# Kernel optimization log

Measured on AMD Instinct MI355X. Metric: run time of the kernel, lower is better.

## Reference

```python
import jax, jax.numpy as jnp
import numpy as np

V, ENC, D, E = 10000, 2048, 512, 512
B, L = 128, 64


def setup_inputs() -> dict:
    key = jax.random.key(0)
    ks = jax.random.split(key, 12)
    s = lambda *sh: 1.0 / np.sqrt(sh[-1])
    return {
        "global_feats": jax.random.normal(ks[0], (B, ENC), jnp.float32),
        "encoded_captions": jax.random.randint(ks[1], (B, L), 0, V, jnp.int64),
        "caption_lengths": jax.random.randint(ks[2], (B,), 1, L, jnp.int64),
        "W_embed": jax.random.normal(ks[3], (V, E), jnp.float32) * 0.02,
        "W_init": jax.random.normal(ks[4], (D, ENC), jnp.float32) * s(ENC),
        "b_init": jnp.zeros((D,), jnp.float32),
        "W_ih": jax.random.normal(ks[5], (3 * D, E), jnp.float32) * s(E),
        "W_hh": jax.random.normal(ks[6], (3 * D, D), jnp.float32) * s(D),
        "b_ih": jnp.zeros((3 * D,), jnp.float32),
        "b_hh": jnp.zeros((3 * D,), jnp.float32),
        "W_fc": jax.random.normal(ks[7], (V, D), jnp.float32) * s(D),
        "b_fc": jnp.zeros((V,), jnp.float32),
    }


def reference(global_feats, encoded_captions, caption_lengths,
              W_embed, W_init, b_init, W_ih, W_hh, b_ih, b_hh, W_fc, b_fc):
    # init_hidden: h0 = tanh(Linear(global_feats))  -> (B, D)
    h0 = jnp.tanh(global_feats @ W_init.T + b_init)

    # teacher forcing over timesteps 0..L-2 (PyTorch GRU gate order: r, z, n)
    emb = W_embed[encoded_captions[:, : L - 1]]          # (B, L-1, E)
    gi = jnp.einsum('ble,ge->blg', emb, W_ih) + b_ih     # (B, L-1, 3D) precomputed input gates
    gi = jnp.swapaxes(gi, 0, 1)                          # (L-1, B, 3D) scan over time

    def step(h, gi_t):
        gh = h @ W_hh.T + b_hh                           # (B, 3D)
        i_r, i_z, i_n = jnp.split(gi_t, 3, axis=-1)
        h_r, h_z, h_n = jnp.split(gh, 3, axis=-1)
        r = jax.nn.sigmoid(i_r + h_r)
        z = jax.nn.sigmoid(i_z + h_z)
        n = jnp.tanh(i_n + r * h_n)
        h_new = (1.0 - z) * n + z * h
        return h_new, h_new

    _, hs = jax.lax.scan(step, h0, gi)                   # hs: (L-1, B, D)
    # dropout is identity in eval/reference mode
    logits = jnp.einsum('lbd,vd->blv', hs, W_fc) + b_fc  # (B, L-1, V)
    return logits, caption_lengths - 1
```

## Files before the change

kernel.cpp:

```cpp
#include <hip/hip_runtime.h>
#include <hip/hip_bf16.h>

#define V_    10000
#define ENC_  2048
#define D_    512
#define B_    128
#define L_    64
#define T_    63
#define M_    (B_ * L_ - B_)
#define G_    (3 * D_)
#define LOGITS_SZ ((long)M_ * V_)
#define SCAN_NB 64

typedef __bf16 bf16x8_t __attribute__((ext_vector_type(8)));
typedef float  f32x4_t  __attribute__((ext_vector_type(4)));
typedef short  s16x8_t  __attribute__((ext_vector_type(8)));
typedef unsigned long long ull_t;

typedef __attribute__((address_space(3))) char*       lds_cptr_t;
typedef const __attribute__((address_space(1))) char* glb_cptr_t;

__device__ __forceinline__ void gload_lds16(const void* g, void* l) {
  __builtin_amdgcn_global_load_lds((glb_cptr_t)g, (lds_cptr_t)l, 16, 0, 0);
}
__device__ __forceinline__ float bf2f(short s) {
  return __uint_as_float(((unsigned)(unsigned short)s) << 16);
}
__device__ __forceinline__ short f2bf(float f) {
  __hip_bfloat16 h = __float2bfloat16(f);
  return *reinterpret_cast<short*>(&h);
}
__device__ __forceinline__ s16x8_t cvt8(const float* p) {
  f32x4_t lo = *reinterpret_cast<const f32x4_t*>(p);
  f32x4_t hi = *reinterpret_cast<const f32x4_t*>(p + 4);
  s16x8_t r;
#pragma unroll
  for (int e = 0; e < 4; e++) { r[e] = f2bf(lo[e]); r[4 + e] = f2bf(hi[e]); }
  return r;
}
__device__ __forceinline__ float sigmoidf_(float x) {
  return 1.0f / (1.0f + __expf(-x));
}
__device__ __forceinline__ bf16x8_t lds_frag(const short* p) {
  return __builtin_bit_cast(bf16x8_t, *reinterpret_cast<const s16x8_t*>(p));
}

__global__ void GG_cvt5(const float* __restrict__ whh, __hip_bfloat16* __restrict__ dwhh,
                        const float* __restrict__ wih, __hip_bfloat16* __restrict__ dwih,
                        const float* __restrict__ wemb, __hip_bfloat16* __restrict__ dwemb,
                        const float* __restrict__ winit, __hip_bfloat16* __restrict__ dwinit,
                        const float* __restrict__ gf, __hip_bfloat16* __restrict__ dgf) {
  const int i = blockIdx.x * blockDim.x + threadIdx.x;
  const float* s; __hip_bfloat16* d; int off;
  if (i < 98304)        { s = whh;   d = dwhh;   off = i; }
  else if (i < 196608)  { s = wih;   d = dwih;   off = i - 98304; }
  else if (i < 836608)  { s = wemb;  d = dwemb;  off = i - 196608; }
  else if (i < 967680)  { s = winit; d = dwinit; off = i - 836608; }
  else                  { s = gf;    d = dgf;    off = i - 967680; }
  s16x8_t v = cvt8(s + (long)off * 8);
  *reinterpret_cast<s16x8_t*>(d + (long)off * 8) = v;
}

__global__ void GG_cvt_kernel(const float* __restrict__ src,
                              __hip_bfloat16* __restrict__ dst, int n8) {
  int i = blockIdx.x * blockDim.x + threadIdx.x;
  if (i < n8) {
    s16x8_t v = cvt8(src + (long)i * 8);
    *reinterpret_cast<s16x8_t*>(dst + (long)i * 8) = v;
  }
}

__global__ __launch_bounds__(256) void GG_gemm_h0(
    const __hip_bfloat16* __restrict__ gfB,
    const __hip_bfloat16* __restrict__ WinitB,
    const float* __restrict__ binit,
    __hip_bfloat16* __restrict__ hfull) {
  __shared__ short sA[128 * 64];
  __shared__ short sB[128 * 64];
  const int lane = threadIdx.x & 63;
  const int wave = threadIdx.x >> 6;
  const int n0 = blockIdx.x * 128;
  const int srow = lane >> 3;
  const int scol = (lane & 7) * 8;

  f32x4_t acc[4][4] = {};

  const __hip_bfloat16* aptr[4];
  const __hip_bfloat16* bptr[4];
#pragma unroll
  for (int i = 0; i < 4; i++) {
    const int r = (wave * 4 + i) * 8 + srow;
    aptr[i] = gfB + (long)r * ENC_ + scol;
    bptr[i] = WinitB + (long)(n0 + r) * ENC_ + scol;
  }

  const int wm = (wave >> 1) * 64;
  const int wn = (wave & 1) * 64;
  const int fr = lane & 15;
  const int fk = (lane >> 4) * 8;

  for (int kt = 0; kt < 32; kt++) {
    __syncthreads();
#pragma unroll
    for (int i = 0; i < 4; i++) {
      const int chunk = wave * 4 + i;
      gload_lds16(aptr[i] + kt * 64, sA + chunk * 512);
      gload_lds16(bptr[i] + kt * 64, sB + chunk * 512);
    }
    __syncthreads();
#pragma unroll
    for (int kk = 0; kk < 2; kk++) {
      bf16x8_t a[4], b[4];
#pragma unroll
      for (int i = 0; i < 4; i++) {
        a[i] = lds_frag(sA + (wm + i * 16 + fr) * 64 + kk * 32 + fk);
        b[i] = lds_frag(sB + (wn + i * 16 + fr) * 64 + kk * 32 + fk);
      }
#pragma unroll
      for (int i = 0; i < 4; i++)
#pragma unroll
        for (int j = 0; j < 4; j++)
          acc[i][j] = __builtin_amdgcn_mfma_f32_16x16x32_bf16(a[i], b[j], acc[i][j], 0, 0, 0);
    }
  }

  const int fq = lane >> 4;
#pragma unroll
  for (int j = 0; j < 4; j++) {
    const int n = n0 + wn + j * 16 + fr;
    const float bv = binit[n];
#pragma unroll
    for (int i = 0; i < 4; i++)
#pragma unroll
      for (int rr = 0; rr < 4; rr++) {
        const int m = wm + i * 16 + fq * 4 + rr;
        hfull[(long)m * 64 * 512 + n] = __float2bfloat16(tanhf(acc[i][j][rr] + bv));
      }
  }
}

__global__ __launch_bounds__(256) void GG_gemm_gi(
    const __hip_bfloat16* __restrict__ WembB,
    const int* __restrict__ cap,
    const __hip_bfloat16* __restrict__ WihB,
    const float* __restrict__ bias,
    __hip_bfloat16* __restrict__ C) {
  __shared__ short sA[128 * 64];
  __shared__ short sB[128 * 64];
  const int lane = threadIdx.x & 63;
  const int wave = threadIdx.x >> 6;
  const int m0 = blockIdx.y * 128;
  const int n0 = blockIdx.x * 128;
  const int srow = lane >> 3;
  const int scol = (lane & 7) * 8;

  f32x4_t acc[4][4] = {};

  const __hip_bfloat16* aptr[4];
  const __hip_bfloat16* bptr[4];
#pragma unroll
  for (int i = 0; i < 4; i++) {
    const int r = (wave * 4 + i) * 8 + srow;
    const int bt = m0 + r;
    const int bb = bt / 63;
    const int tt = bt - bb * 63;
    aptr[i] = WembB + (long)cap[bb * L_ + tt] * 512 + scol;
    bptr[i] = WihB + (long)(n0 + r) * 512 + scol;
  }

  const int wm = (wave >> 1) * 64;
  const int wn = (wave & 1) * 64;
  const int fr = lane & 15;
  const int fk = (lane >> 4) * 8;

  for (int kt = 0; kt < 8; kt++) {
    __syncthreads();
#pragma unroll
    for (int i = 0; i < 4; i++) {
      const int chunk = wave * 4 + i;
      gload_lds16(aptr[i] + kt * 64, sA + chunk * 512);
      gload_lds16(bptr[i] + kt * 64, sB + chunk * 512);
    }
    __syncthreads();
#pragma unroll
    for (int kk = 0; kk < 2; kk++) {
      bf16x8_t a[4], b[4];
#pragma unroll
      for (int i = 0; i < 4; i++) {
        a[i] = lds_frag(sA + (wm + i * 16 + fr) * 64 + kk * 32 + fk);
        b[i] = lds_frag(sB + (wn + i * 16 + fr) * 64 + kk * 32 + fk);
      }
#pragma unroll
      for (int i = 0; i < 4; i++)
#pragma unroll
        for (int j = 0; j < 4; j++)
          acc[i][j] = __builtin_amdgcn_mfma_f32_16x16x32_bf16(a[i], b[j], acc[i][j], 0, 0, 0);
    }
  }

  const int fq = lane >> 4;
#pragma unroll
  for (int j = 0; j < 4; j++) {
    const int n = n0 + wn + j * 16 + fr;
    const float bv = bias[n];
#pragma unroll
    for (int i = 0; i < 4; i++)
#pragma unroll
      for (int rr = 0; rr < 4; rr++) {
        const int m = m0 + wm + i * 16 + fq * 4 + rr;
        C[(long)m * G_ + n] = __float2bfloat16(acc[i][j][rr] + bv);
      }
  }
}

template <bool BBF16>
__global__ __launch_bounds__(512) void GG_gemm_logits(
    const __hip_bfloat16* __restrict__ hfull,
    const void* __restrict__ Bsrc,
    const float* __restrict__ bias,
    float* __restrict__ C) {
  const int flat = blockIdx.x;
  const int xcd = flat & 7;
  const int s = flat >> 3;
  const int col = xcd * 5 + s % 5;
  const int row = s / 5;
  const int m0 = row * 128;
  const int n0 = col * 256;

  __shared__ short sA[128 * 64];
  __shared__ short sB[256 * 64];
  const int lane = threadIdx.x & 63;
  const int wave = threadIdx.x >> 6;
  const int srow = lane >> 3;
  const int scol = (lane & 7) * 8;

  f32x4_t acc[4][4] = {};

  const __hip_bfloat16* aptr[2];
#pragma unroll
  for (int i = 0; i < 2; i++) {
    const int r = (wave + i * 8) * 8 + srow;
    const int m = m0 + r;
    const int bb = m / 63;
    const int tt = m - bb * 63;
    aptr[i] = hfull + ((long)bb * 64 + tt + 1) * 512 + scol;
  }
  const __hip_bfloat16* bptrB[4];
  const float* bptrF[4];
#pragma unroll
  for (int i = 0; i < 4; i++) {
    int nrow = n0 + (wave + i * 8) * 8 + srow;
    nrow = (nrow < V_) ? nrow : (V_ - 1);
    if constexpr (BBF16) bptrB[i] = (const __hip_bfloat16*)Bsrc + (long)nrow * 512 + scol;
    else                 bptrF[i] = (const float*)Bsrc + (long)nrow * 512 + scol;
  }

  const int wm = (wave >> 2) * 64;
  const int wn = (wave & 3) * 64;
  const int fr = lane & 15;
  const int fk = (lane >> 4) * 8;

  for (int kt = 0; kt < 8; kt++) {
    s16x8_t vb[4];
    if constexpr (!BBF16) {
#pragma unroll
      for (int i = 0; i < 4; i++) vb[i] = cvt8(bptrF[i] + kt * 64);
    }
    __syncthreads();
#pragma unroll
    for (int i = 0; i < 2; i++)
      gload_lds16(aptr[i] + kt * 64, sA + (wave + i * 8) * 512);
#pragma unroll
    for (int i = 0; i < 4; i++) {
      if constexpr (BBF16)
        gload_lds16(bptrB[i] + kt * 64, sB + (wave + i * 8) * 512);
      else
        *reinterpret_cast<s16x8_t*>(sB + (wave + i * 8) * 512 + lane * 8) = vb[i];
    }
    __syncthreads();
#pragma unroll
    for (int kk = 0; kk < 2; kk++) {
      bf16x8_t a[4], b[4];
#pragma unroll
      for (int i = 0; i < 4; i++) {
        a[i] = lds_frag(sA + (wm + i * 16 + fr) * 64 + kk * 32 + fk);
        b[i] = lds_frag(sB + (wn + i * 16 + fr) * 64 + kk * 32 + fk);
      }
#pragma unroll
      for (int i = 0; i < 4; i++)
#pragma unroll
        for (int j = 0; j < 4; j++)
          acc[i][j] = __builtin_amdgcn_mfma_f32_16x16x32_bf16(a[i], b[j], acc[i][j], 0, 0, 0);
    }
  }

  const int fq = lane >> 4;
#pragma unroll
  for (int j = 0; j < 4; j++) {
    const int n = n0 + wn + j * 16 + fr;
    if (n >= V_) continue;
    const float bv = bias[n];
#pragma unroll
    for (int i = 0; i < 4; i++)
#pragma unroll
      for (int rr = 0; rr < 4; rr++) {
        const int m = m0 + wm + i * 16 + fq * 4 + rr;
        C[(long)m * V_ + n] = acc[i][j][rr] + bv;
      }
  }
}

__global__ __launch_bounds__(256) void GG_scan_persist(
    __hip_bfloat16* __restrict__ hfull,
    const __hip_bfloat16* __restrict__ gi,
    const __hip_bfloat16* __restrict__ WhhB,
    const float* __restrict__ bhh,
    int* __restrict__ flagbase) {
  __shared__ short sW[48 * 512];
  const int lane = threadIdx.x & 63;
  const int wave = threadIdx.x >> 6;
  const int strip = blockIdx.x & 31;
  const int half  = blockIdx.x >> 5;
  const int d0 = strip * 16;
  const int fr = lane & 15;
  const int g4 = lane >> 4;
  int* myflags = flagbase + half * 32;

  for (int rr = wave; rr < 48; rr += 4) {
    const int grow = (rr >> 4) * 512 + d0 + (rr & 15);
    gload_lds16(WhhB + (long)grow * 512 + (lane ^ (rr & 7)) * 8, sW + rr * 512);
  }

  const int dd = d0 + fr;
  const int bbase = half * 64 + wave * 16 + g4 * 4;
  const float br_ = bhh[dd], bz_ = bhh[512 + dd], bn_ = bhh[1024 + dd];
  const short* gis = (const short*)gi;

  const int arow = half * 64 + wave * 16 + fr;
  const ull_t abase0 =
      (ull_t)hfull + ((ull_t)arow * 64 * 512 + (unsigned)(g4 * 8)) * 2ull;

  ull_t sbase[4];
  const short* gp0[4];
#pragma unroll
  for (int rr = 0; rr < 4; rr++) {
    sbase[rr] = (ull_t)hfull +
                ((ull_t)(bbase + rr) * 64 * 512 + (unsigned)dd) * 2ull;
    gp0[rr] = gis + (long)(bbase + rr) * T_ * G_ + dd;
  }

  unsigned cr[4], cz[4], cn[4];
  float hp[4];
#pragma unroll
  for (int rr = 0; rr < 4; rr++) {
    cr[rr] = (unsigned short)gp0[rr][0];
    cz[rr] = (unsigned short)gp0[rr][512];
    cn[rr] = (unsigned short)gp0[rr][1024];
    hp[rr] = bf2f(*(const short*)&hfull[((long)(bbase + rr) * 64) * 512 + dd]);
  }

  asm volatile("s_waitcnt vmcnt(0)" ::: "memory");
  __syncthreads();

  for (int t = 0; t < T_; t++) {
    if (t > 0) {
      while (true) {
        const int v = __hip_atomic_load(&myflags[lane & 31], __ATOMIC_RELAXED,
                                        __HIP_MEMORY_SCOPE_SYSTEM);
        if (__all(v >= t)) break;
        __builtin_amdgcn_s_sleep(1);
      }
    }

    const ull_t ab = abase0 + (ull_t)t * 1024ull;
    f32x4_t a[16];
#define ALOAD(IDX, OFF)                                                        \
    asm volatile("global_load_dwordx4 %0, %1, off offset:" #OFF " sc0 sc1"     \
                 : "=v"(a[IDX]) : "v"(ab));
    ALOAD(0, 0)    ALOAD(1, 64)   ALOAD(2, 128)  ALOAD(3, 192)
    ALOAD(4, 256)  ALOAD(5, 320)  ALOAD(6, 384)  ALOAD(7, 448)
    ALOAD(8, 512)  ALOAD(9, 576)  ALOAD(10, 640) ALOAD(11, 704)
    ALOAD(12, 768) ALOAD(13, 832) ALOAD(14, 896) ALOAD(15, 960)
#undef ALOAD

    const int tp = (t < T_ - 1) ? (t + 1) : (T_ - 1);
    unsigned nr[4], nz[4], nn[4];
#pragma unroll
    for (int rr = 0; rr < 4; rr++) {
      const short* gp = gp0[rr] + (long)tp * G_;
      asm volatile("global_load_ushort %0, %1, off"             : "=v"(nr[rr]) : "v"(gp));
      asm volatile("global_load_ushort %0, %1, off offset:1024" : "=v"(nz[rr]) : "v"(gp));
      asm volatile("global_load_ushort %0, %1, off offset:2048" : "=v"(nn[rr]) : "v"(gp));
    }

    asm volatile("s_waitcnt vmcnt(12)" ::: "memory");
    __builtin_amdgcn_sched_barrier(0);

    f32x4_t acc[3] = {};
#pragma unroll
    for (int kt = 0; kt < 16; kt++) {
      const bf16x8_t afr = __builtin_bit_cast(bf16x8_t, a[kt]);
      const int gsw = ((kt * 4 + g4) ^ (fr & 7)) * 8;
      bf16x8_t bfr[3];
#pragma unroll
      for (int j = 0; j < 3; j++) bfr[j] = lds_frag(sW + (j * 16 + fr) * 512 + gsw);
#pragma unroll
      for (int j = 0; j < 3; j++)
        acc[j] = __builtin_amdgcn_mfma_f32_16x16x32_bf16(afr, bfr[j], acc[j], 0, 0, 0);
    }

#pragma unroll
    for (int rr = 0; rr < 4; rr++) {
      const float rg = sigmoidf_(bf2f((short)cr[rr]) + acc[0][rr] + br_);
      const float zg = sigmoidf_(bf2f((short)cz[rr]) + acc[1][rr] + bz_);
      const float ng = tanhf(bf2f((short)cn[rr]) + rg * (acc[2][rr] + bn_));
      const short hnb = f2bf((1.f - zg) * ng + zg * hp[rr]);
      hp[rr] = bf2f(hnb);
      const ull_t saddr = sbase[rr] + (ull_t)(t + 1) * 1024ull;
      const unsigned int val = (unsigned short)hnb;
      asm volatile("global_store_short %0, %1, off sc0 sc1"
                   :: "v"(saddr), "v"(val) : "memory");
    }

    asm volatile("s_waitcnt vmcnt(0)" ::: "memory");
    __builtin_amdgcn_sched_barrier(0);
#pragma unroll
    for (int rr = 0; rr < 4; rr++) { cr[rr] = nr[rr]; cz[rr] = nz[rr]; cn[rr] = nn[rr]; }

    if (t < T_ - 1) {
      __syncthreads();
      if (threadIdx.x == 0)
        __hip_atomic_store(&myflags[strip], t + 1, __ATOMIC_RELAXED,
                           __HIP_MEMORY_SCOPE_SYSTEM);
    }
  }
}

__global__ void GG_tail_kernel(const int* __restrict__ lens, float* __restrict__ out) {
  const int b = threadIdx.x;
  if (b < B_) out[LOGITS_SZ + b] = (float)(lens[b] - 1);
}

extern "C" void kernel_launch(void* const* d_in, const int* in_sizes, int n_in,
                              void* d_out, int out_size, void* d_ws, size_t ws_size,
                              hipStream_t stream) {
  const float* gf      = (const float*)d_in[0];
  const int*   cap     = (const int*)d_in[1];
  const int*   lens    = (const int*)d_in[2];
  const float* W_embed = (const float*)d_in[3];
  const float* W_init  = (const float*)d_in[4];
  const float* b_init  = (const float*)d_in[5];
  const float* W_ih    = (const float*)d_in[6];
  const float* W_hh    = (const float*)d_in[7];
  const float* b_ih    = (const float*)d_in[8];
  const float* b_hh    = (const float*)d_in[9];
  const float* W_fc    = (const float*)d_in[10];
  const float* b_fc    = (const float*)d_in[11];
  float* out = (float*)d_out;

  char* ob = (char*)d_out;
  __hip_bfloat16* gi_ws  = (__hip_bfloat16*)ob;
  __hip_bfloat16* WhhB   = (__hip_bfloat16*)(ob + 25165824);
  __hip_bfloat16* WihB   = (__hip_bfloat16*)(ob + 27262976);
  __hip_bfloat16* WembB  = (__hip_bfloat16*)(ob + 29360128);
  __hip_bfloat16* WinitB = (__hip_bfloat16*)(ob + 40894464);
  __hip_bfloat16* gfB    = (__hip_bfloat16*)(ob + 43253760);

  __hip_bfloat16* hfull = (__hip_bfloat16*)d_ws;
  __hip_bfloat16* WfcB  = (__hip_bfloat16*)((char*)d_ws + 8388608);
  const bool big_ws = ws_size >= (size_t)(8388608 + 10240000 + 256);
  int* flags = (int*)((char*)d_ws + (big_ws ? 18628608 : 8388608));

  hipMemsetAsync(flags, 0, 256, stream);

  GG_cvt5<<<dim3(3908), 256, 0, stream>>>(W_hh, WhhB, W_ih, WihB, W_embed, WembB,
                                          W_init, WinitB, gf, gfB);
  if (big_ws)
    GG_cvt_kernel<<<dim3((V_ * D_ / 8 + 255) / 256), 256, 0, stream>>>(W_fc, WfcB, V_ * D_ / 8);

  GG_gemm_h0<<<dim3(4), 256, 0, stream>>>(gfB, WinitB, b_init, hfull);

  GG_gemm_gi<<<dim3(G_ / 128, M_ / 128), 256, 0, stream>>>(WembB, cap, WihB, b_ih, gi_ws);

  GG_scan_persist<<<dim3(SCAN_NB), 256, 0, stream>>>(hfull, gi_ws, WhhB, b_hh, flags);

  if (big_ws)
    GG_gemm_logits<true><<<dim3(2520), 512, 0, stream>>>(hfull, WfcB, b_fc, out);
  else
    GG_gemm_logits<false><<<dim3(2520), 512, 0, stream>>>(hfull, W_fc, b_fc, out);

  GG_tail_kernel<<<dim3(1), 128, 0, stream>>>(lens, out);
}
```

Baseline: 543.2 us.

## XOR-swizzle LDS tiles in GEMMs and fold W_fc conversion into one kernel

Applies an XOR swizzle to the 16-byte column chunks of the LDS tiles in the h0, gi and logits GEMMs. Global-to-LDS loads write permuted chunks and fragment reads use the matching XOR index, which is meant to cut LDS bank conflicts on the MFMA fragment reads. It also merges the separate W_fc fp32-to-bf16 conversion launch into the existing multi-tensor conversion kernel, saving one launch. The swizzle must line up exactly between writers and readers on both the gload_lds and the register-store paths.

```diff
diff --git a/kernel.cpp b/kernel.cpp
--- a/kernel.cpp
+++ b/kernel.cpp
@@ -45,29 +45,25 @@
   return __builtin_bit_cast(bf16x8_t, *reinterpret_cast<const s16x8_t*>(p));
 }
 
-__global__ void GG_cvt5(const float* __restrict__ whh, __hip_bfloat16* __restrict__ dwhh,
+__global__ void GG_cvt6(const float* __restrict__ whh, __hip_bfloat16* __restrict__ dwhh,
                         const float* __restrict__ wih, __hip_bfloat16* __restrict__ dwih,
                         const float* __restrict__ wemb, __hip_bfloat16* __restrict__ dwemb,
                         const float* __restrict__ winit, __hip_bfloat16* __restrict__ dwinit,
-                        const float* __restrict__ gf, __hip_bfloat16* __restrict__ dgf) {
+                        const float* __restrict__ gf, __hip_bfloat16* __restrict__ dgf,
+                        const float* __restrict__ wfc, __hip_bfloat16* __restrict__ dwfc) {
   const int i = blockIdx.x * blockDim.x + threadIdx.x;
   const float* s; __hip_bfloat16* d; int off;
   if (i < 98304)        { s = whh;   d = dwhh;   off = i; }
   else if (i < 196608)  { s = wih;   d = dwih;   off = i - 98304; }
   else if (i < 836608)  { s = wemb;  d = dwemb;  off = i - 196608; }
   else if (i < 967680)  { s = winit; d = dwinit; off = i - 836608; }
-  else                  { s = gf;    d = dgf;    off = i - 967680; }
+  else if (i < 1000448) { s = gf;    d = dgf;    off = i - 967680; }
+  else {
+    if (dwfc == nullptr || i >= 1640448) return;
+    s = wfc; d = dwfc; off = i - 1000448;
+  }
   s16x8_t v = cvt8(s + (long)off * 8);
   *reinterpret_cast<s16x8_t*>(d + (long)off * 8) = v;
-}
-
-__global__ void GG_cvt_kernel(const float* __restrict__ src,
-                              __hip_bfloat16* __restrict__ dst, int n8) {
-  int i = blockIdx.x * blockDim.x + threadIdx.x;
-  if (i < n8) {
-    s16x8_t v = cvt8(src + (long)i * 8);
-    *reinterpret_cast<s16x8_t*>(dst + (long)i * 8) = v;
-  }
 }
 
 __global__ __launch_bounds__(256) void GG_gemm_h0(
@@ -81,7 +77,7 @@
   const int wave = threadIdx.x >> 6;
   const int n0 = blockIdx.x * 128;
   const int srow = lane >> 3;
-  const int scol = (lane & 7) * 8;
+  const int scolz = ((lane & 7) ^ (srow & 7)) * 8;
 
   f32x4_t acc[4][4] = {};
 
@@ -90,14 +86,14 @@
 #pragma unroll
   for (int i = 0; i < 4; i++) {
     const int r = (wave * 4 + i) * 8 + srow;
-    aptr[i] = gfB + (long)r * ENC_ + scol;
-    bptr[i] = WinitB + (long)(n0 + r) * ENC_ + scol;
+    aptr[i] = gfB + (long)r * ENC_ + scolz;
+    bptr[i] = WinitB + (long)(n0 + r) * ENC_ + scolz;
   }
 
   const int wm = (wave >> 1) * 64;
   const int wn = (wave & 1) * 64;
   const int fr = lane & 15;
-  const int fk = (lane >> 4) * 8;
+  const int g4 = lane >> 4;
 
   for (int kt = 0; kt < 32; kt++) {
     __syncthreads();
@@ -110,11 +106,12 @@
     __syncthreads();
 #pragma unroll
     for (int kk = 0; kk < 2; kk++) {
+      const int gsw = ((kk * 4 + g4) ^ (fr & 7)) * 8;
       bf16x8_t a[4], b[4];
 #pragma unroll
       for (int i = 0; i < 4; i++) {
-        a[i] = lds_frag(sA + (wm + i * 16 + fr) * 64 + kk * 32 + fk);
-        b[i] = lds_frag(sB + (wn + i * 16 + fr) * 64 + kk * 32 + fk);
+        a[i] = lds_frag(sA + (wm + i * 16 + fr) * 64 + gsw);
+        b[i] = lds_frag(sB + (wn + i * 16 + fr) * 64 + gsw);
       }
 #pragma unroll
       for (int i = 0; i < 4; i++)
@@ -152,7 +149,7 @@
   const int m0 = blockIdx.y * 128;
   const int n0 = blockIdx.x * 128;
   const int srow = lane >> 3;
-  const int scol = (lane & 7) * 8;
+  const int scolz = ((lane & 7) ^ (srow & 7)) * 8;
 
   f32x4_t acc[4][4] = {};
 
@@ -164,14 +161,14 @@
     const int bt = m0 + r;
     const int bb = bt / 63;
     const int tt = bt - bb * 63;
-    aptr[i] = WembB + (long)cap[bb * L_ + tt] * 512 + scol;
-    bptr[i] = WihB + (long)(n0 + r) * 512 + scol;
+    aptr[i] = WembB + (long)cap[bb * L_ + tt] * 512 + scolz;
+    bptr[i] = WihB + (long)(n0 + r) * 512 + scolz;
   }
 
   const int wm = (wave >> 1) * 64;
   const int wn = (wave & 1) * 64;
   const int fr = lane & 15;
-  const int fk = (lane >> 4) * 8;
+  const int g4 = lane >> 4;
 
   for (int kt = 0; kt < 8; kt++) {
     __syncthreads();
@@ -184,11 +181,12 @@
     __syncthreads();
 #pragma unroll
     for (int kk = 0; kk < 2; kk++) {
+      const int gsw = ((kk * 4 + g4) ^ (fr & 7)) * 8;
       bf16x8_t a[4], b[4];
 #pragma unroll
       for (int i = 0; i < 4; i++) {
-        a[i] = lds_frag(sA + (wm + i * 16 + fr) * 64 + kk * 32 + fk);
-        b[i] = lds_frag(sB + (wn + i * 16 + fr) * 64 + kk * 32 + fk);
+        a[i] = lds_frag(sA + (wm + i * 16 + fr) * 64 + gsw);
+        b[i] = lds_frag(sB + (wn + i * 16 + fr) * 64 + gsw);
       }
 #pragma unroll
       for (int i = 0; i < 4; i++)
@@ -232,7 +230,8 @@
   const int lane = threadIdx.x & 63;
   const int wave = threadIdx.x >> 6;
   const int srow = lane >> 3;
-  const int scol = (lane & 7) * 8;
+  const int scol  = (lane & 7) * 8;
+  const int scolz = ((lane & 7) ^ (srow & 7)) * 8;
 
   f32x4_t acc[4][4] = {};
 
@@ -243,7 +242,7 @@
     const int m = m0 + r;
     const int bb = m / 63;
     const int tt = m - bb * 63;
-    aptr[i] = hfull + ((long)bb * 64 + tt + 1) * 512 + scol;
+    aptr[i] = hfull + ((long)bb * 64 + tt + 1) * 512 + scolz;
   }
   const __hip_bfloat16* bptrB[4];
   const float* bptrF[4];
@@ -251,14 +250,14 @@
   for (int i = 0; i < 4; i++) {
     int nrow = n0 + (wave + i * 8) * 8 + srow;
     nrow = (nrow < V_) ? nrow : (V_ - 1);
-    if constexpr (BBF16) bptrB[i] = (const __hip_bfloat16*)Bsrc + (long)nrow * 512 + scol;
+    if constexpr (BBF16) bptrB[i] = (const __hip_bfloat16*)Bsrc + (long)nrow * 512 + scolz;
     else                 bptrF[i] = (const float*)Bsrc + (long)nrow * 512 + scol;
   }
 
   const int wm = (wave >> 2) * 64;
   const int wn = (wave & 3) * 64;
   const int fr = lane & 15;
-  const int fk = (lane >> 4) * 8;
+  const int g4 = lane >> 4;
 
   for (int kt = 0; kt < 8; kt++) {
     s16x8_t vb[4];
@@ -275,16 +274,18 @@
       if constexpr (BBF16)
         gload_lds16(bptrB[i] + kt * 64, sB + (wave + i * 8) * 512);
       else
-        *reinterpret_cast<s16x8_t*>(sB + (wave + i * 8) * 512 + lane * 8) = vb[i];
+        *reinterpret_cast<s16x8_t*>(
+            sB + (wave + i * 8) * 512 + srow * 64 + (((lane & 7) ^ (srow & 7)) * 8)) = vb[i];
     }
     __syncthreads();
 #pragma unroll
     for (int kk = 0; kk < 2; kk++) {
+      const int gsw = ((kk * 4 + g4) ^ (fr & 7)) * 8;
       bf16x8_t a[4], b[4];
 #pragma unroll
       for (int i = 0; i < 4; i++) {
-        a[i] = lds_frag(sA + (wm + i * 16 + fr) * 64 + kk * 32 + fk);
-        b[i] = lds_frag(sB + (wn + i * 16 + fr) * 64 + kk * 32 + fk);
+        a[i] = lds_frag(sA + (wm + i * 16 + fr) * 64 + gsw);
+        b[i] = lds_frag(sB + (wn + i * 16 + fr) * 64 + gsw);
       }
 #pragma unroll
       for (int i = 0; i < 4; i++)
@@ -473,10 +474,9 @@
 
   hipMemsetAsync(flags, 0, 256, stream);
 
-  GG_cvt5<<<dim3(3908), 256, 0, stream>>>(W_hh, WhhB, W_ih, WihB, W_embed, WembB,
-                                          W_init, WinitB, gf, gfB);
-  if (big_ws)
-    GG_cvt_kernel<<<dim3((V_ * D_ / 8 + 255) / 256), 256, 0, stream>>>(W_fc, WfcB, V_ * D_ / 8);
+  GG_cvt6<<<dim3(6408), 256, 0, stream>>>(W_hh, WhhB, W_ih, WihB, W_embed, WembB,
+                                          W_init, WinitB, gf, gfB,
+                                          W_fc, big_ws ? WfcB : nullptr);
 
   GG_gemm_h0<<<dim3(4), 256, 0, stream>>>(gfB, WinitB, b_init, hfull);
 
```

Result: faster. 516.7 us (-4.9%).
